# Kernel optimization log

Measured on AMD Instinct MI355X. Metric: run time of the kernel, lower is better.

## Reference

```python
import jax, jax.numpy as jnp
import numpy as np

N = 32768          # flattened tokens
D = 256            # latent_dim
K = 8192           # codebook_size
COMMIT_W = 0.25    # commitment_weight


def setup_inputs() -> dict:
    key = jax.random.key(0)
    k1, k2, k3 = jax.random.split(key, 3)
    x = jax.random.normal(k1, (N, D), dtype=jnp.float32)
    # nn.init.uniform_(embedding.weight, -1/K, 1/K)
    embedding = jax.random.uniform(k2, (K, D), dtype=jnp.float32,
                                   minval=-1.0 / K, maxval=1.0 / K)
    # out_proj: Linear(D, D, bias=False); torch default kaiming-uniform ~ U(-1/sqrt(D), 1/sqrt(D))
    lim = 1.0 / np.sqrt(D)
    w_out = jax.random.uniform(k3, (D, D), dtype=jnp.float32, minval=-lim, maxval=lim)
    return {"x": x, "embedding": embedding, "w_out": w_out}


def reference(x, embedding, w_out):
    sg = jax.lax.stop_gradient
    # codebook = out_proj(embedding.weight)  -> [K, D]
    codebook = embedding @ w_out.T
    # torch.cdist(x, codebook, p=2) is only consumed by argmin, so squared
    # Euclidean distances give the identical ids without the sqrt.
    x2 = jnp.sum(x * x, axis=1, keepdims=True)          # [N, 1]
    c2 = jnp.sum(codebook * codebook, axis=1)           # [K]
    dists = x2 - 2.0 * (x @ codebook.T) + c2            # [N, K]
    ids = jnp.argmin(dists, axis=1)                     # [N]
    q = codebook[ids]                                   # [N, D] gather
    # straight-through estimator
    quantized = x + sg(q - x)
    loss = jnp.mean((x - sg(quantized)) ** 2) \
         + COMMIT_W * jnp.mean((quantized - sg(x)) ** 2)
    return quantized, ids, loss
```

## Files before the change

### kernel.cpp

```cpp
#include <hip/hip_runtime.h>
#include <hip/hip_bf16.h>

#define N_TOK 32768
#define DIM   256
#define KCB   8192
#define CAP   64
#define MARGIN 1.75e-4f

typedef __attribute__((ext_vector_type(8))) short short8v;
typedef __attribute__((ext_vector_type(4))) float f32x4;

__device__ __forceinline__ unsigned int mono_f32(float f) {
    unsigned int u = __float_as_uint(f);
    return (u >> 31) ? ~u : (u | 0x80000000u);
}
__device__ __forceinline__ float invmono_f32(unsigned int m) {
    unsigned int u = (m & 0x80000000u) ? (m & 0x7FFFFFFFu) : ~m;
    return __uint_as_float(u);
}
__device__ __forceinline__ unsigned long long shfl_xor_u64(unsigned long long v, int m) {
    unsigned int lo = (unsigned int)v, hi = (unsigned int)(v >> 32);
    lo = __shfl_xor(lo, m, 64);
    hi = __shfl_xor(hi, m, 64);
    return ((unsigned long long)hi << 32) | lo;
}
__device__ __forceinline__ void gl_lds16(const void* g, void* l) {
    __builtin_amdgcn_global_load_lds(
        (const __attribute__((address_space(1))) unsigned int*)g,
        (__attribute__((address_space(3))) unsigned int*)l, 16, 0, 0);
}
__device__ __forceinline__ unsigned int rne16(float f) {
    unsigned int b = __float_as_uint(f);
    return (b + 0x7FFFu + ((b >> 16) & 1u)) >> 16;
}

__global__ __launch_bounds__(256) void transpose_w(const float* __restrict__ w,
                                                   float* __restrict__ wT) {
    __shared__ float tile[32][33];
    int bx = blockIdx.x & 7, by = blockIdx.x >> 3;
    int x0 = bx * 32, y0 = by * 32;
    int tx = threadIdx.x & 31, ty = threadIdx.x >> 5;
    #pragma unroll
    for (int i = 0; i < 32; i += 8)
        tile[ty + i][tx] = w[(y0 + ty + i) * DIM + x0 + tx];
    __syncthreads();
    #pragma unroll
    for (int i = 0; i < 32; i += 8)
        wT[(x0 + ty + i) * DIM + y0 + tx] = tile[tx][ty + i];
}

#define KPB 8
__global__ __launch_bounds__(256) void build_codebook(const float* __restrict__ emb,
                                                      const float* __restrict__ wT,
                                                      float* __restrict__ cb) {
    __shared__ float e[KPB][DIM];
    const int k0 = blockIdx.x * KPB;
    const int t = threadIdx.x;
    for (int i = t; i < KPB * DIM / 4; i += 256)
        ((float4*)&e[0][0])[i] = ((const float4*)(emb + (size_t)k0 * DIM))[i];
    __syncthreads();
    const int d = t;
    float acc[KPB];
    #pragma unroll
    for (int kk = 0; kk < KPB; ++kk) acc[kk] = 0.f;
    for (int j = 0; j < DIM; ++j) {
        float w = wT[j * DIM + d];
        #pragma unroll
        for (int kk = 0; kk < KPB; ++kk)
            acc[kk] = fmaf(e[kk][j], w, acc[kk]);
    }
    #pragma unroll
    for (int kk = 0; kk < KPB; ++kk)
        cb[(size_t)(k0 + kk) * DIM + d] = acc[kk];
}

__global__ __launch_bounds__(256) void sumsq_np_bf(const float* __restrict__ a,
                                                   float* __restrict__ out,
                                                   uint4* __restrict__ bfout) {
    #pragma clang fp contract(off)
    int idx = blockIdx.x * 256 + threadIdx.x;
    int r = idx >> 1, h = idx & 1;
    const float* b = a + (size_t)r * DIM + h * 128;
    uint4* dst = bfout ? bfout + ((size_t)r * 32 + h * 16) : (uint4*)0;
    float r0 = 0.f, r1 = 0.f, r2 = 0.f, r3 = 0.f,
          r4 = 0.f, r5 = 0.f, r6 = 0.f, r7 = 0.f;
    #pragma unroll
    for (int i = 0; i < 128; i += 8) {
        float4 p = *(const float4*)(b + i);
        float4 q = *(const float4*)(b + i + 4);
        if (bfout) {
            uint4 u;
            u.x = rne16(p.x) | (rne16(p.y) << 16);
            u.y = rne16(p.z) | (rne16(p.w) << 16);
            u.z = rne16(q.x) | (rne16(q.y) << 16);
            u.w = rne16(q.z) | (rne16(q.w) << 16);
            dst[i >> 3] = u;
        }
        r0 = r0 + p.x * p.x; r1 = r1 + p.y * p.y;
        r2 = r2 + p.z * p.z; r3 = r3 + p.w * p.w;
        r4 = r4 + q.x * q.x; r5 = r5 + q.y * q.y;
        r6 = r6 + q.z * q.z; r7 = r7 + q.w * q.w;
    }
    float half = ((r0 + r1) + (r2 + r3)) + ((r4 + r5) + (r6 + r7));
    float other = __shfl_xor(half, 1, 64);
    if (h == 0) out[r] = half + other;
}

__global__ __launch_bounds__(512, 4) void score_collect(
    const unsigned short* __restrict__ xbf,
    const unsigned short* __restrict__ cbbf,
    unsigned int* __restrict__ gmax,
    unsigned int* __restrict__ ccnt,
    unsigned short* __restrict__ cand)
{
    __shared__ unsigned char lds[51200];
    float* auxm = (float*)(lds + 49152);
    const int t = threadIdx.x;
    const int l = t & 63, w = t >> 6;
    const int g = l >> 4, c = l & 15;
    const int wr = w >> 2, wc = w & 3;
    const int bid = blockIdx.x;
    const int xcd = bid & 7, idx = bid >> 3;
    const int bx = xcd + 8 * (idx & 31);
    const int by = idx >> 5;
    const int row0 = bx * 128;
    const int col0 = by * 256;

    f32x4 acc[4][4];
    #pragma unroll
    for (int m = 0; m < 4; ++m)
        #pragma unroll
        for (int n = 0; n < 4; ++n) acc[m][n] = (f32x4){0.f, 0.f, 0.f, 0.f};

    const char* xg = (const char*)xbf  + (size_t)row0 * 512;
    const char* cg = (const char*)cbbf + (size_t)col0 * 512;

#define STAGE(buf, ks)                                                         \
    do {                                                                       \
        const int kb_ = (ks) * 64;                                             \
        unsigned char* la_ = lds + (buf) * 24576;                              \
        {                   \
            int row_ = t >> 2, pc_ = t & 3;                                    \
            int sz_ = (row_ >> 1) & 3;                                         \
            gl_lds16(xg + (size_t)row_ * 512 + kb_ + ((pc_ ^ sz_) * 16),       \
                     la_ + t * 16);                                            \
        }                                                                      \
        _Pragma("unroll")                                                      \
        for (int r_ = 0; r_ < 2; ++r_) {    \
            int i_ = r_ * 512 + t;                                             \
            int row_ = i_ >> 2, pc_ = i_ & 3;                                  \
            int sz_ = (row_ >> 1) & 3;                                         \
            gl_lds16(cg + (size_t)row_ * 512 + kb_ + ((pc_ ^ sz_) * 16),       \
                     la_ + 8192 + i_ * 16);                                    \
        }                                                                      \
    } while (0)

#define COMPUTE(buf)                                                           \
    do {                                                                       \
        const unsigned char* la_ = lds + (buf) * 24576;                        \
        const unsigned char* lb_ = la_ + 8192;                                 \
        const int swq_ = (g ^ ((c >> 1) & 3)) * 16;                            \
        short8v af[4], bv[4];                                                  \
        _Pragma("unroll")                                                      \
        for (int m = 0; m < 4; ++m)                                            \
            af[m] = *(const short8v*)(la_ + (64 * wr + 16 * m + c) * 64 + swq_); \
        _Pragma("unroll")                                                      \
        for (int n = 0; n < 4; ++n)                                            \
            bv[n] = *(const short8v*)(lb_ + (64 * wc + 16 * n + c) * 64 + swq_); \
        _Pragma("unroll")                                                      \
        for (int m = 0; m < 4; ++m)                                            \
            _Pragma("unroll")                                                  \
            for (int n = 0; n < 4; ++n)                                        \
                acc[m][n] = __builtin_amdgcn_mfma_f32_16x16x32_bf16(           \
                    af[m], bv[n], acc[m][n], 0, 0, 0);                         \
    } while (0)

    STAGE(0, 0);
    asm volatile("s_waitcnt vmcnt(0)" ::: "memory");
    __syncthreads();

    #pragma unroll
    for (int s = 0; s < 8; ++s) {
        if (s < 7) STAGE((s + 1) & 1, s + 1);
        COMPUTE(s & 1);
        asm volatile("s_waitcnt vmcnt(0)" ::: "memory");
        __syncthreads();
    }
#undef STAGE
#undef COMPUTE

    #pragma unroll
    for (int m = 0; m < 4; ++m)
        #pragma unroll
        for (int j = 0; j < 4; ++j) {
            float v = acc[m][0][j];
            #pragma unroll
            for (int n = 1; n < 4; ++n) v = fmaxf(v, acc[m][n][j]);
            #pragma unroll
            for (int msk = 1; msk < 16; msk <<= 1)
                v = fmaxf(v, __shfl_xor(v, msk, 64));
            if (c == 0) auxm[wc * 128 + 64 * wr + 16 * m + 4 * g + j] = v;
        }
    __syncthreads();

    if (t < 128) {
        float vm = fmaxf(fmaxf(auxm[t], auxm[128 + t]),
                         fmaxf(auxm[256 + t], auxm[384 + t]));
        unsigned int ou = atomicMax(&gmax[row0 + t], mono_f32(vm));
        auxm[t] = fmaxf(vm, invmono_f32(ou));
    }
    __syncthreads();

    #pragma unroll
    for (int m = 0; m < 4; ++m)
        #pragma unroll
        for (int j = 0; j < 4; ++j) {
            int lrow = 64 * wr + 16 * m + 4 * g + j;
            float thr = auxm[lrow] - MARGIN;
            #pragma unroll
            for (int n = 0; n < 4; ++n) {
                float s = acc[m][n][j];
                if (s >= thr) {
                    int row = row0 + lrow;
                    unsigned int idx2 = atomicAdd(&ccnt[row], 1u);
                    if (idx2 < CAP)
                        cand[((size_t)row << 6) + idx2] =
                            (unsigned short)(col0 + 64 * wc + 16 * n + c);
                }
            }
        }
}

__device__ __forceinline__ unsigned long long np_dist_pack(
    const float4* __restrict__ xr4, const float* __restrict__ cb,
    int k, float X2, const float* __restrict__ c2)
{
    #pragma clang fp contract(off)
    const float4* cr4 = (const float4*)(cb + (size_t)k * DIM);
    float a = 0.f;
    #pragma unroll 8
    for (int t4 = 0; t4 < DIM / 4; ++t4) {
        float4 xv = xr4[t4];
        float4 cv = cr4[t4];
        a = fmaf(xv.x, cv.x, a);
        a = fmaf(xv.y, cv.y, a);
        a = fmaf(xv.z, cv.z, a);
        a = fmaf(xv.w, cv.w, a);
    }
    float u  = X2 - 2.0f * a;
    float dd = u + c2[k];
    return ((unsigned long long)mono_f32(dd) << 32) | (unsigned int)k;
}

__global__ __launch_bounds__(256) void exact_select(
    const float* __restrict__ x, const float* __restrict__ cb,
    const float* __restrict__ x2, const float* __restrict__ c2,
    const unsigned int* __restrict__ ccnt, const unsigned short* __restrict__ cand,
    unsigned long long* __restrict__ best)
{
    const int l = threadIdx.x & 63;
    const int row = (blockIdx.x * 256 + threadIdx.x) >> 6;
    const unsigned int cnt = ccnt[row];
    const float4* xr4 = (const float4*)(x + (size_t)row * DIM);
    const float X2 = x2[row];
    unsigned long long bp = ~0ull;

    if (cnt <= CAP) {
        if (l < (int)cnt) {
            int k = (int)cand[((size_t)row << 6) + l];
            bp = np_dist_pack(xr4, cb, k, X2, c2);
        }
    } else {
        for (int k = l; k < KCB; k += 64) {
            unsigned long long pk = np_dist_pack(xr4, cb, k, X2, c2);
            if (pk < bp) bp = pk;
        }
    }
    #pragma unroll
    for (int m = 1; m < 64; m <<= 1) {
        unsigned long long v = shfl_xor_u64(bp, m);
        if (v < bp) bp = v;
    }
    if (l == 0) best[row] = bp;
}

__global__ __launch_bounds__(256, 4) void score_argmin(const float* __restrict__ x,
                                                       const float* __restrict__ cb,
                                                       const float* __restrict__ c2,
                                                       const float* __restrict__ x2,
                                                       unsigned long long* __restrict__ best) {
    #pragma clang fp contract(off)
    __shared__ float As[16][128];
    __shared__ float Bs[16][128];
    const int row0 = blockIdx.x * 128;
    const int col0 = blockIdx.y * 128;
    const int t = threadIdx.x;
    const int tn = t & 15, tm = t >> 4;
    const int lrow = t >> 1, lseg = (t & 1) * 4;
    float acc[8][8];
    #pragma unroll
    for (int i = 0; i < 8; ++i)
        #pragma unroll
        for (int j = 0; j < 8; ++j) acc[i][j] = 0.f;
    const float* xp = x  + (size_t)(row0 + lrow) * DIM + lseg;
    const float* cp = cb + (size_t)(col0 + lrow) * DIM + lseg;
    for (int k0 = 0; k0 < DIM; k0 += 16) {
        float4 a0 = *(const float4*)(xp + k0);
        float4 a1 = *(const float4*)(xp + k0 + 8);
        float4 b0 = *(const float4*)(cp + k0);
        float4 b1 = *(const float4*)(cp + k0 + 8);
        __syncthreads();
        As[lseg + 0][lrow] = a0.x; As[lseg + 1][lrow] = a0.y;
        As[lseg + 2][lrow] = a0.z; As[lseg + 3][lrow] = a0.w;
        As[8 + lseg + 0][lrow] = a1.x; As[8 + lseg + 1][lrow] = a1.y;
        As[8 + lseg + 2][lrow] = a1.z; As[8 + lseg + 3][lrow] = a1.w;
        Bs[lseg + 0][lrow] = b0.x; Bs[lseg + 1][lrow] = b0.y;
        Bs[lseg + 2][lrow] = b0.z; Bs[lseg + 3][lrow] = b0.w;
        Bs[8 + lseg + 0][lrow] = b1.x; Bs[8 + lseg + 1][lrow] = b1.y;
        Bs[8 + lseg + 2][lrow] = b1.z; Bs[8 + lseg + 3][lrow] = b1.w;
        __syncthreads();
        #pragma unroll
        for (int kk = 0; kk < 16; ++kk) {
            float a[8], b[8];
            *(float4*)(a)     = *(const float4*)&As[kk][tm * 4];
            *(float4*)(a + 4) = *(const float4*)&As[kk][64 + tm * 4];
            *(float4*)(b)     = *(const float4*)&Bs[kk][tn * 4];
            *(float4*)(b + 4) = *(const float4*)&Bs[kk][64 + tn * 4];
            #pragma unroll
            for (int i = 0; i < 8; ++i)
                #pragma unroll
                for (int j = 0; j < 8; ++j)
                    acc[i][j] = fmaf(a[i], b[j], acc[i][j]);
        }
    }
    float c2v[8], x2v[8];
    #pragma unroll
    for (int j = 0; j < 4; ++j) {
        c2v[j]     = c2[col0 + tn * 4 + j];
        c2v[4 + j] = c2[col0 + 64 + tn * 4 + j];
    }
    #pragma unroll
    for (int i = 0; i < 4; ++i) {
        x2v[i]     = x2[row0 + tm * 4 + i];
        x2v[4 + i] = x2[row0 + 64 + tm * 4 + i];
    }
    #pragma unroll
    for (int i = 0; i < 8; ++i) {
        unsigned long long bp = ~0ull;
        #pragma unroll
        for (int j = 0; j < 8; ++j) {
            float tt = 2.0f * acc[i][j];
            float u  = x2v[i] - tt;
            float dd = u + c2v[j];
            int id = col0 + ((j < 4) ? (tn * 4 + j) : (64 + tn * 4 + (j - 4)));
            unsigned long long pk = ((unsigned long long)mono_f32(dd) << 32) | (unsigned int)id;
            if (pk < bp) bp = pk;
        }
        #pragma unroll
        for (int m = 1; m < 16; m <<= 1) {
            unsigned long long v = shfl_xor_u64(bp, m);
            if (v < bp) bp = v;
        }
        if (tn == 0) {
            int gr = row0 + ((i < 4) ? (tm * 4 + i) : (64 + tm * 4 + (i - 4)));
            atomicMin(&best[gr], bp);
        }
    }
}

__global__ __launch_bounds__(256) void finalize(const float* __restrict__ x,
                                                const float* __restrict__ cb,
                                                const unsigned long long* __restrict__ best,
                                                float* __restrict__ out,
                                                float* __restrict__ partial) {
    __shared__ float rsum[16];
    const int t = threadIdx.x;
    const int rloc = t >> 4, seg = t & 15;
    const int r = blockIdx.x * 16 + rloc;
    const int id = (int)(best[r] & 0xFFFFFFFFu);
    const float4* xp = (const float4*)(x  + (size_t)r  * DIM) + seg * 4;
    const float4* cp = (const float4*)(cb + (size_t)id * DIM) + seg * 4;
    float4*       op = (float4*)(out + (size_t)r * DIM) + seg * 4;
    float s = 0.f;
    #pragma unroll
    for (int i = 0; i < 4; ++i) {
        float4 xv = xp[i], qv = cp[i];
        op[i] = qv;
        float dx = xv.x - qv.x, dy = xv.y - qv.y;
        float dz = xv.z - qv.z, dw = xv.w - qv.w;
        s += dx * dx + dy * dy + dz * dz + dw * dw;
    }
    #pragma unroll
    for (int m = 1; m < 16; m <<= 1) s += __shfl_xor(s, m, 64);
    if (seg == 0) {
        rsum[rloc] = s;
        out[(size_t)N_TOK * DIM + r] = (float)id;
    }
    __syncthreads();
    if (t == 0) {
        float bs = 0.f;
        #pragma unroll
        for (int i = 0; i < 16; ++i) bs += rsum[i];
        partial[blockIdx.x] = bs;
    }
}

__global__ __launch_bounds__(256) void reduce_loss(const float* __restrict__ partial,
                                                   float* __restrict__ out) {
    float s = 0.f;
    for (int i = threadIdx.x; i < 2048 / 4; i += 256) {
        float4 v = ((const float4*)partial)[i];
        s += (v.x + v.y) + (v.z + v.w);
    }
    #pragma unroll
    for (int o = 32; o > 0; o >>= 1) s += __shfl_down(s, o, 64);
    __shared__ float w4[4];
    if ((threadIdx.x & 63) == 0) w4[threadIdx.x >> 6] = s;
    __syncthreads();
    if (threadIdx.x == 0)
        out[(size_t)N_TOK * DIM + N_TOK] =
            (w4[0] + w4[1] + w4[2] + w4[3]) * (1.25f / ((float)N_TOK * (float)DIM));
}

extern "C" void kernel_launch(void* const* d_in, const int* in_sizes, int n_in,
                              void* d_out, int out_size, void* d_ws, size_t ws_size,
                              hipStream_t stream) {
    const float* x     = (const float*)d_in[0];
    const float* emb   = (const float*)d_in[1];
    const float* w_out = (const float*)d_in[2];
    float* out = (float*)d_out;

    char* ws = (char*)d_ws;
    unsigned long long* best = (unsigned long long*)ws;
    float* x2 = (float*)(ws + 262400);
    float* wT = (float*)(ws + 393472);
    float* cb = (float*)(ws + 655616);
    float* c2 = (float*)(ws + 9044224);
    unsigned int*   gmax = (unsigned int*)(ws + 9076992);
    unsigned int*   ccnt = (unsigned int*)(ws + 9208064);
    unsigned short* cand = (unsigned short*)(ws + 9339136);
    unsigned short* xbf  = (unsigned short*)(ws + 13533440);
    unsigned short* cbbf = (unsigned short*)(ws + 30310656);
    float* partial = wT;
    const size_t NEED = 34504960;
    const bool useMfma = (ws_size >= NEED);

    transpose_w   <<<64,  256, 0, stream>>>(w_out, wT);
    build_codebook<<<KCB / KPB, 256, 0, stream>>>(emb, wT, cb);
    sumsq_np_bf   <<<N_TOK * 2 / 256, 256, 0, stream>>>(x, x2,
                      useMfma ? (uint4*)xbf : (uint4*)0);
    sumsq_np_bf   <<<KCB * 2 / 256, 256, 0, stream>>>(cb, c2,
                      useMfma ? (uint4*)cbbf : (uint4*)0);

    if (useMfma) {
        hipMemsetAsync(gmax, 0, 262144, stream);
        score_collect <<<8192, 512, 0, stream>>>(xbf, cbbf, gmax, ccnt, cand);
        exact_select  <<<N_TOK / 4, 256, 0, stream>>>(x, cb, x2, c2, ccnt, cand, best);
    } else {
        hipMemsetAsync(best, 0xFF, 262144, stream);
        score_argmin  <<<dim3(N_TOK / 128, KCB / 128), 256, 0, stream>>>(x, cb, c2, x2, best);
    }

    finalize      <<<N_TOK / 16, 256, 0, stream>>>(x, cb, best, out, partial);
    reduce_loss   <<<1, 256, 0, stream>>>(partial, out);
}
```

Before: 463.5 us.

## Fuse preprocessing and select/finalize kernels, raise wave priority around MFMA

```diff
diff --git a/kernel.cpp b/kernel.cpp
--- a/kernel.cpp
+++ b/kernel.cpp
@@ -34,19 +34,51 @@
     return (b + 0x7FFFu + ((b >> 16) & 1u)) >> 16;
 }
 
-__global__ __launch_bounds__(256) void transpose_w(const float* __restrict__ w,
-                                                   float* __restrict__ wT) {
+__global__ __launch_bounds__(256) void fused_pre(const float* __restrict__ w,
+                                                 float* __restrict__ wT,
+                                                 const float* __restrict__ x,
+                                                 float* __restrict__ x2,
+                                                 uint4* __restrict__ xbf) {
+    #pragma clang fp contract(off)
     __shared__ float tile[32][33];
-    int bx = blockIdx.x & 7, by = blockIdx.x >> 3;
-    int x0 = bx * 32, y0 = by * 32;
-    int tx = threadIdx.x & 31, ty = threadIdx.x >> 5;
-    #pragma unroll
-    for (int i = 0; i < 32; i += 8)
-        tile[ty + i][tx] = w[(y0 + ty + i) * DIM + x0 + tx];
-    __syncthreads();
-    #pragma unroll
-    for (int i = 0; i < 32; i += 8)
-        wT[(x0 + ty + i) * DIM + y0 + tx] = tile[tx][ty + i];
+    const int t = threadIdx.x;
+    if (blockIdx.x < 64) {
+        int bx = blockIdx.x & 7, by = blockIdx.x >> 3;
+        int x0 = bx * 32, y0 = by * 32;
+        int tx = t & 31, ty = t >> 5;
+        #pragma unroll
+        for (int i = 0; i < 32; i += 8)
+            tile[ty + i][tx] = w[(y0 + ty + i) * DIM + x0 + tx];
+        __syncthreads();
+        #pragma unroll
+        for (int i = 0; i < 32; i += 8)
+            wT[(x0 + ty + i) * DIM + y0 + tx] = tile[tx][ty + i];
+        return;
+    }
+    int idx = (blockIdx.x - 64) * 256 + t;
+    int r = idx >> 1, h = idx & 1;
+    const float* b = x + (size_t)r * DIM + h * 128;
+    uint4* dst = xbf + ((size_t)r * 32 + h * 16);
+    float r0 = 0.f, r1 = 0.f, r2 = 0.f, r3 = 0.f,
+          r4 = 0.f, r5 = 0.f, r6 = 0.f, r7 = 0.f;
+    #pragma unroll
+    for (int i = 0; i < 128; i += 8) {
+        float4 p = *(const float4*)(b + i);
+        float4 q = *(const float4*)(b + i + 4);
+        uint4 u;
+        u.x = rne16(p.x) | (rne16(p.y) << 16);
+        u.y = rne16(p.z) | (rne16(p.w) << 16);
+        u.z = rne16(q.x) | (rne16(q.y) << 16);
+        u.w = rne16(q.z) | (rne16(q.w) << 16);
+        dst[i >> 3] = u;
+        r0 = r0 + p.x * p.x; r1 = r1 + p.y * p.y;
+        r2 = r2 + p.z * p.z; r3 = r3 + p.w * p.w;
+        r4 = r4 + q.x * q.x; r5 = r5 + q.y * q.y;
+        r6 = r6 + q.z * q.z; r7 = r7 + q.w * q.w;
+    }
+    float half = ((r0 + r1) + (r2 + r3)) + ((r4 + r5) + (r6 + r7));
+    float other = __shfl_xor(half, 1, 64);
+    if (h == 0) x2[r] = half + other;
 }
 
 #define KPB 8
@@ -167,12 +199,14 @@
         _Pragma("unroll")                                                      \
         for (int n = 0; n < 4; ++n)                                            \
             bv[n] = *(const short8v*)(lb_ + (64 * wc + 16 * n + c) * 64 + swq_); \
+        __builtin_amdgcn_s_setprio(1);                                         \
         _Pragma("unroll")                                                      \
         for (int m = 0; m < 4; ++m)                                            \
             _Pragma("unroll")                                                  \
             for (int n = 0; n < 4; ++n)                                        \
                 acc[m][n] = __builtin_amdgcn_mfma_f32_16x16x32_bf16(           \
                     af[m], bv[n], acc[m][n], 0, 0, 0);                         \
+        __builtin_amdgcn_s_setprio(0);                                         \
     } while (0)
 
     STAGE(0, 0);
@@ -252,14 +286,16 @@
     return ((unsigned long long)mono_f32(dd) << 32) | (unsigned int)k;
 }
 
-__global__ __launch_bounds__(256) void exact_select(
+__global__ __launch_bounds__(256) void select_finalize(
     const float* __restrict__ x, const float* __restrict__ cb,
     const float* __restrict__ x2, const float* __restrict__ c2,
     const unsigned int* __restrict__ ccnt, const unsigned short* __restrict__ cand,
-    unsigned long long* __restrict__ best)
+    float* __restrict__ out, float* __restrict__ partial)
 {
-    const int l = threadIdx.x & 63;
-    const int row = (blockIdx.x * 256 + threadIdx.x) >> 6;
+    __shared__ float wsum[4];
+    const int t = threadIdx.x;
+    const int l = t & 63, wv = t >> 6;
+    const int row = blockIdx.x * 4 + wv;
     const unsigned int cnt = ccnt[row];
     const float4* xr4 = (const float4*)(x + (size_t)row * DIM);
     const float X2 = x2[row];
@@ -281,7 +317,24 @@
         unsigned long long v = shfl_xor_u64(bp, m);
         if (v < bp) bp = v;
     }
-    if (l == 0) best[row] = bp;
+    const int id = (int)(bp & 0xFFFFFFFFu);
+
+    const float4* cp = (const float4*)(cb + (size_t)id * DIM);
+    float4*       op = (float4*)(out + (size_t)row * DIM);
+    float4 xv = xr4[l], qv = cp[l];
+    op[l] = qv;
+    float dx = xv.x - qv.x, dy = xv.y - qv.y;
+    float dz = xv.z - qv.z, dw = xv.w - qv.w;
+    float s = dx * dx + dy * dy + dz * dz + dw * dw;
+    #pragma unroll
+    for (int m = 1; m < 64; m <<= 1) s += __shfl_xor(s, m, 64);
+    if (l == 0) {
+        out[(size_t)N_TOK * DIM + row] = (float)id;
+        wsum[wv] = s;
+    }
+    __syncthreads();
+    if (t == 0)
+        partial[blockIdx.x] = (wsum[0] + wsum[1]) + (wsum[2] + wsum[3]);
 }
 
 __global__ __launch_bounds__(256, 4) void score_argmin(const float* __restrict__ x,
@@ -406,9 +459,9 @@
 }
 
 __global__ __launch_bounds__(256) void reduce_loss(const float* __restrict__ partial,
-                                                   float* __restrict__ out) {
+                                                   int n, float* __restrict__ out) {
     float s = 0.f;
-    for (int i = threadIdx.x; i < 2048 / 4; i += 256) {
+    for (int i = threadIdx.x; i < n / 4; i += 256) {
         float4 v = ((const float4*)partial)[i];
         s += (v.x + v.y) + (v.z + v.w);
     }
@@ -445,22 +498,21 @@
     const size_t NEED = 34504960;
     const bool useMfma = (ws_size >= NEED);
 
-    transpose_w   <<<64,  256, 0, stream>>>(w_out, wT);
-    build_codebook<<<KCB / KPB, 256, 0, stream>>>(emb, wT, cb);
-    sumsq_np_bf   <<<N_TOK * 2 / 256, 256, 0, stream>>>(x, x2,
-                      useMfma ? (uint4*)xbf : (uint4*)0);
-    sumsq_np_bf   <<<KCB * 2 / 256, 256, 0, stream>>>(cb, c2,
-                      useMfma ? (uint4*)cbbf : (uint4*)0);
-
     if (useMfma) {
         hipMemsetAsync(gmax, 0, 262144, stream);
+        fused_pre     <<<64 + N_TOK * 2 / 256, 256, 0, stream>>>(w_out, wT, x, x2, (uint4*)xbf);
+        build_codebook<<<KCB / KPB, 256, 0, stream>>>(emb, wT, cb);
+        sumsq_np_bf   <<<KCB * 2 / 256, 256, 0, stream>>>(cb, c2, (uint4*)cbbf);
         score_collect <<<8192, 512, 0, stream>>>(xbf, cbbf, gmax, ccnt, cand);
-        exact_select  <<<N_TOK / 4, 256, 0, stream>>>(x, cb, x2, c2, ccnt, cand, best);
+        select_finalize<<<N_TOK / 4, 256, 0, stream>>>(x, cb, x2, c2, ccnt, cand, out, partial);
+        reduce_loss   <<<1, 256, 0, stream>>>(partial, N_TOK / 4, out);
     } else {
         hipMemsetAsync(best, 0xFF, 262144, stream);
+        fused_pre     <<<64 + N_TOK * 2 / 256, 256, 0, stream>>>(w_out, wT, x, x2, (uint4*)xbf);
+        build_codebook<<<KCB / KPB, 256, 0, stream>>>(emb, wT, cb);
+        sumsq_np_bf   <<<KCB * 2 / 256, 256, 0, stream>>>(cb, c2, (uint4*)0);
         score_argmin  <<<dim3(N_TOK / 128, KCB / 128), 256, 0, stream>>>(x, cb, c2, x2, best);
-    }
-
-    finalize      <<<N_TOK / 16, 256, 0, stream>>>(x, cb, best, out, partial);
-    reduce_loss   <<<1, 256, 0, stream>>>(partial, out);
-}
+        finalize      <<<N_TOK / 16, 256, 0, stream>>>(x, cb, best, out, partial);
+        reduce_loss   <<<1, 256, 0, stream>>>(partial, N_TOK / 16, out);
+    }
+}
```

Result: faster. 434.5 us (-6.3%).
